# Optimization experiments

Measured on AMD Instinct MI355X. Metric: run time of the kernel, lower is better.

## Reference

```python
import jax, jax.numpy as jnp
import numpy as np
import math

D_MODEL = 1024
N_HEADS = 16
HEAD_DIM = D_MODEL // N_HEADS
B, T = 2, 2048


def _rope(q, k):
    # q, k: (B, H, T, Dh)
    Dh = q.shape[-1]
    Tq = q.shape[2]
    dim = jnp.arange(0, Dh, 2, dtype=jnp.float32)
    inv_freq = 1.0 / (10000.0 ** (dim / Dh))
    pos = jnp.arange(Tq, dtype=jnp.float32)
    freqs = pos[:, None] * inv_freq[None, :]          # (T, Dh/2)
    sin = jnp.sin(freqs)[None, None]                  # (1,1,T,Dh/2)
    cos = jnp.cos(freqs)[None, None]

    def rot(t):
        te, to = t[..., ::2], t[..., 1::2]
        re = te * cos - to * sin
        ro = te * sin + to * cos
        return jnp.stack([re, ro], axis=-1).reshape(t.shape)

    return rot(q), rot(k)


def setup_inputs() -> dict:
    key = jax.random.key(0)
    ks = jax.random.split(key, 4)
    std = 1.0 / math.sqrt(D_MODEL)
    x = jax.random.normal(ks[0], (B, T, D_MODEL), dtype=jnp.float32)
    W_qkv = jax.random.normal(ks[1], (D_MODEL, 3 * D_MODEL), dtype=jnp.float32) * std
    b_qkv = jnp.zeros((3 * D_MODEL,), dtype=jnp.float32)
    W_out = jax.random.normal(ks[2], (D_MODEL, D_MODEL), dtype=jnp.float32) * std
    b_out = jnp.zeros((D_MODEL,), dtype=jnp.float32)
    attention_mask = jnp.ones((B, T), dtype=jnp.int32)
    return {"x": x, "attention_mask": attention_mask, "W_qkv": W_qkv,
            "b_qkv": b_qkv, "W_out": W_out, "b_out": b_out}


def reference(x, attention_mask, W_qkv, b_qkv, W_out, b_out):
    Bx, Tx, D = x.shape
    qkv = x @ W_qkv + b_qkv                            # (B,T,3D)
    q, k, v = jnp.split(qkv, 3, axis=-1)
    # (B,T,H,Dh) -> (B,H,T,Dh)
    q = q.reshape(Bx, Tx, N_HEADS, HEAD_DIM).transpose(0, 2, 1, 3)
    k = k.reshape(Bx, Tx, N_HEADS, HEAD_DIM).transpose(0, 2, 1, 3)
    v = v.reshape(Bx, Tx, N_HEADS, HEAD_DIM).transpose(0, 2, 1, 3)
    q, k = _rope(q, k)
    scale = 1.0 / math.sqrt(float(HEAD_DIM))
    scores = jnp.einsum('bhqd,bhkd->bhqk', q, k) * scale
    causal = jnp.tril(jnp.ones((Tx, Tx), dtype=bool))[None, None]
    pad = attention_mask.astype(bool)[:, None, None, :]
    mask = causal & pad
    scores = jnp.where(mask, scores, -jnp.inf)
    probs = jax.nn.softmax(scores, axis=-1)
    out = jnp.einsum('bhqk,bhkd->bhqd', probs, v)      # (B,H,T,Dh)
    out = out.transpose(0, 2, 1, 3).reshape(Bx, Tx, D)
    return out @ W_out + b_out
```

## Files before the change

### kernel.cpp

```cpp
#include <hip/hip_runtime.h>
#include <math.h>
#include <stdint.h>

#define D_MODEL 1024
#define N_HEADS 16
#define HEAD_DIM 64
#define BATCH 2
#define SEQ 2048
#define TOKENS (BATCH * SEQ)

typedef __attribute__((ext_vector_type(8))) short short8;
typedef __attribute__((ext_vector_type(8))) _Float16 half8;
typedef __attribute__((ext_vector_type(4))) float floatx4;

#define BMFMA(a, b, c) __builtin_amdgcn_mfma_f32_16x16x32_bf16(a, b, c, 0, 0, 0)
#define HMFMA(a, b, c) __builtin_amdgcn_mfma_f32_16x16x32_f16(a, b, c, 0, 0, 0)

__device__ __forceinline__ unsigned short f2bf(float f) {
    uint32_t u = __float_as_uint(f);
    u += 0x7fffu + ((u >> 16) & 1u);
    return (unsigned short)(u >> 16);
}
__device__ __forceinline__ float bf2f(unsigned short h) {
    return __uint_as_float(((uint32_t)h) << 16);
}
__device__ __forceinline__ unsigned short f2h(float f) {
    union { _Float16 h; unsigned short u; } cv;
    cv.h = (_Float16)f;
    return cv.u;
}
__device__ __forceinline__ float h2f(unsigned short u) {
    union { unsigned short u; _Float16 h; } cv;
    cv.u = u;
    return (float)cv.h;
}

#define GLD_LDS16(gp, lp) __builtin_amdgcn_global_load_lds(                 \
    (const __attribute__((address_space(1))) void*)(gp),                    \
    (__attribute__((address_space(3))) void*)(lp), 16, 0, 0)

__global__ __launch_bounds__(256) void split_inputs(
    const float* __restrict__ X, const float* __restrict__ Wqkv,
    const float* __restrict__ Wout, const int* __restrict__ am,
    unsigned short* __restrict__ Axh, unsigned short* __restrict__ Bt,
    unsigned short* __restrict__ Bt2, unsigned long long* __restrict__ mbits,
    float2* __restrict__ tab)
{
    __shared__ float t[32][33];
    const int tid = threadIdx.x;
    const int bid = blockIdx.x;
    if (bid < 2048) {
        const int idx = bid * 2048 + tid * 8;
        const int row = idx >> 10;
        const int c = idx & 1023;
        float4 v0 = *(const float4*)(X + (size_t)row * 1024 + c);
        float4 v1 = *(const float4*)(X + (size_t)row * 1024 + c + 4);
        float f[8] = {v0.x, v0.y, v0.z, v0.w, v1.x, v1.y, v1.z, v1.w};
        uint32_t p[4];
#pragma unroll
        for (int j = 0; j < 4; ++j)
            p[j] = (uint32_t)f2h(f[2 * j]) | ((uint32_t)f2h(f[2 * j + 1]) << 16);
        *(uint4*)(Axh + (size_t)row * 1024 + c) = *(uint4*)p;
    } else if (bid < 5120) {
        const int id = bid - 2048;
        const int n0 = (id % 96) * 32, k0 = (id / 96) * 32;
        const int c = tid & 31, r = tid >> 5;
#pragma unroll
        for (int i = 0; i < 4; ++i)
            t[r + 8 * i][c] = Wqkv[(size_t)(k0 + r + 8 * i) * 3072 + n0 + c];
        __syncthreads();
#pragma unroll
        for (int i = 0; i < 4; ++i) {
            int dn = r + 8 * i;
            Bt[(size_t)(n0 + dn) * 1024 + k0 + c] = f2h(t[c][dn]);
        }
    } else if (bid < 6144) {
        const int id = bid - 5120;
        const int n0 = (id & 31) * 32, k0 = (id >> 5) * 32;
        const int c = tid & 31, r = tid >> 5;
#pragma unroll
        for (int i = 0; i < 4; ++i)
            t[r + 8 * i][c] = Wout[(size_t)(k0 + r + 8 * i) * 1024 + n0 + c];
        __syncthreads();
#pragma unroll
        for (int i = 0; i < 4; ++i) {
            int dn = r + 8 * i;
            Bt2[(size_t)(n0 + dn) * 1024 + k0 + c] = f2h(t[c][dn]);
        }
    } else if (bid == 6144) {
        if (tid < 64) {
            const int* a = am + tid * 64;
            unsigned long long m = 0ull;
            for (int j = 0; j < 64; ++j)
                m |= (unsigned long long)(a[j] != 0 ? 1u : 0u) << j;
            mbits[tid] = m;
        }
    } else {
        const int i = bid - 6145;
#pragma unroll
        for (int e = 0; e < 16; ++e) {
            int idx = i * 4096 + e * 256 + tid;
            int tt = idx >> 5, pr = idx & 31;
            double ex = (double)(2 * pr) / 64.0;
            float inv = (float)exp2(-ex * 13.287712379549449);
            float ang = (float)tt * inv;
            float s, c;
            __sincosf(ang, &s, &c);
            tab[idx] = make_float2(c, s);
        }
    }
}

__global__ __launch_bounds__(256) void gemm_qkv_fused(
    const unsigned short* __restrict__ Axh, const unsigned short* __restrict__ Bt,
    const float* __restrict__ bias, const float2* __restrict__ tab,
    unsigned short* __restrict__ Qh, unsigned short* __restrict__ Kh,
    unsigned short* __restrict__ Vh)
{
    __shared__ __align__(16) unsigned short sA0[4096], sA1[4096];
    __shared__ __align__(16) unsigned short sB0[4096], sB1[4096];

    const int tid = threadIdx.x;
    const int w = tid >> 6, lane = tid & 63;
    const int l15 = lane & 15, quad = lane >> 4;
    const int wm = w >> 1, wn = w & 1;

    const int lin = blockIdx.x;
    const int msuper = lin / 192;
    const int rem = lin % 192;
    const int m0 = (msuper * 8 + (rem & 7)) * 128;
    const int n0 = (rem >> 3) * 128;

    const int ch = (lane & 3) ^ ((lane >> 3) & 3);
    const int sw = (quad ^ ((l15 >> 1) & 3)) * 8;

    const unsigned short* aG[2];
    const unsigned short* bG[2];
#pragma unroll
    for (int i = 0; i < 2; ++i) {
        aG[i] = Axh + (size_t)(m0 + (w * 2 + i) * 16 + (lane >> 2)) * 1024 + ch * 8;
        bG[i] = Bt + (size_t)(n0 + (w * 2 + i) * 16 + (lane >> 2)) * 1024 + ch * 8;
    }

    floatx4 acc[4][4];
#pragma unroll
    for (int fm = 0; fm < 4; ++fm)
#pragma unroll
        for (int fn = 0; fn < 4; ++fn) acc[fm][fn] = (floatx4)0.f;

    for (int ks = 0; ks < 16; ++ks) {
        const int ko = ks * 64;
        __syncthreads();
#pragma unroll
        for (int i = 0; i < 2; ++i) {
            GLD_LDS16(aG[i] + ko,      sA0 + (w * 2 + i) * 512);
            GLD_LDS16(aG[i] + ko + 32, sA1 + (w * 2 + i) * 512);
            GLD_LDS16(bG[i] + ko,      sB0 + (w * 2 + i) * 512);
            GLD_LDS16(bG[i] + ko + 32, sB1 + (w * 2 + i) * 512);
        }
        __syncthreads();

        half8 a0[4], a1[4], b0[4], b1[4];
#pragma unroll
        for (int fm = 0; fm < 4; ++fm) {
            const int off = ((wm * 4 + fm) * 16 + l15) * 32 + sw;
            a0[fm] = *(const half8*)&sA0[off];
            a1[fm] = *(const half8*)&sA1[off];
        }
#pragma unroll
        for (int fn = 0; fn < 4; ++fn) {
            const int off = ((wn * 4 + fn) * 16 + l15) * 32 + sw;
            b0[fn] = *(const half8*)&sB0[off];
            b1[fn] = *(const half8*)&sB1[off];
        }
#pragma unroll
        for (int fm = 0; fm < 4; ++fm)
#pragma unroll
            for (int fn = 0; fn < 4; ++fn) {
                floatx4 a = acc[fm][fn];
                a = HMFMA(a0[fm], b0[fn], a);
                a = HMFMA(a1[fm], b1[fn], a);
                acc[fm][fn] = a;
            }
    }

    if (n0 < 2048) {
        const bool isQ = (n0 < 1024);
        unsigned short* dst = isQ ? Qh : Kh;
        const float qs = isQ ? 0.125f : 1.0f;
#pragma unroll
        for (int fm = 0; fm < 4; ++fm)
#pragma unroll
            for (int fn = 0; fn < 4; ++fn) {
                const int col = n0 + (wn * 4 + fn) * 16 + l15;
                const int hcol = col & 1023;
                const int hh = hcol >> 6, d = hcol & 63;
                const int pr = d >> 1;
                const bool odd = (d & 1) != 0;
                const float bv = bias[col];
#pragma unroll
                for (int r = 0; r < 4; ++r) {
                    const int row = m0 + (wm * 4 + fm) * 16 + quad * 4 + r;
                    const int tg = row & 2047, bb = row >> 11;
                    float val = acc[fm][fn][r] + bv;
                    float part = __shfl_xor(val, 1);
                    const float2 cs = tab[tg * 32 + pr];
                    float res = odd ? (part * cs.y + val * cs.x)
                                    : (val * cs.x - part * cs.y);
                    dst[((size_t)(bb * 16 + hh) * SEQ + tg) * 64 + d] =
                        f2h(res * qs);
                }
            }
    } else {
#pragma unroll
        for (int fm = 0; fm < 4; ++fm)
#pragma unroll
            for (int fn = 0; fn < 4; ++fn) {
                const int col = n0 + (wn * 4 + fn) * 16 + l15;
                const int hcol = col & 1023;
                const int hh = hcol >> 6, d = hcol & 63;
                const float bv = bias[col];
                const int row0 = m0 + (wm * 4 + fm) * 16 + quad * 4;
                const int tg0 = row0 & 2047, bb = row0 >> 11;
                uint32_t pk0 = (uint32_t)f2bf(acc[fm][fn][0] + bv)
                             | ((uint32_t)f2bf(acc[fm][fn][1] + bv) << 16);
                uint32_t pk1 = (uint32_t)f2bf(acc[fm][fn][2] + bv)
                             | ((uint32_t)f2bf(acc[fm][fn][3] + bv) << 16);
                *(uint2*)(Vh + ((size_t)(bb * 16 + hh) * 64 + d) * SEQ + tg0) =
                    make_uint2(pk0, pk1);
            }
    }
}

template<int WM, int WN, int FM, int FN>
__global__ __launch_bounds__(256) void gemm_mfma_h(
    const unsigned short* __restrict__ A, int lda,
    const unsigned short* __restrict__ Bt, int ldb,
    const float* __restrict__ bias, float* __restrict__ C, int ldc, int nTiles)
{
    constexpr int BM = WM * FM * 16;
    constexpr int BN = WN * FN * 16;
    constexpr int NA = BM / 64;
    constexpr int NB = BN / 64;

    __shared__ __align__(16) unsigned short sA0[BM * 32];
    __shared__ __align__(16) unsigned short sA1[BM * 32];
    __shared__ __align__(16) unsigned short sB0[BN * 32];
    __shared__ __align__(16) unsigned short sB1[BN * 32];

    const int tid = threadIdx.x;
    const int w = tid >> 6, lane = tid & 63;
    const int l15 = lane & 15, quad = lane >> 4;
    const int wm = w / WN, wn = w % WN;

    const int lin = blockIdx.x;
    const int msuper = lin / (8 * nTiles);
    const int rem = lin % (8 * nTiles);
    const int m0 = (msuper * 8 + (rem & 7)) * BM;
    const int n0 = (rem >> 3) * BN;

    const int ch = (lane & 3) ^ ((lane >> 3) & 3);
    const int sw = (quad ^ ((l15 >> 1) & 3)) * 8;

    const unsigned short* aG[NA];
    const unsigned short* bG[NB];
#pragma unroll
    for (int i = 0; i < NA; ++i)
        aG[i] = A + (size_t)(m0 + (w * NA + i) * 16 + (lane >> 2)) * lda + ch * 8;
#pragma unroll
    for (int i = 0; i < NB; ++i)
        bG[i] = Bt + (size_t)(n0 + (w * NB + i) * 16 + (lane >> 2)) * ldb + ch * 8;

    floatx4 acc[FM][FN];
#pragma unroll
    for (int fm = 0; fm < FM; ++fm)
#pragma unroll
        for (int fn = 0; fn < FN; ++fn) acc[fm][fn] = (floatx4)0.f;

    for (int ks = 0; ks < 16; ++ks) {
        const int ko = ks * 64;
        __syncthreads();
#pragma unroll
        for (int i = 0; i < NA; ++i) {
            GLD_LDS16(aG[i] + ko,      sA0 + (w * NA + i) * 512);
            GLD_LDS16(aG[i] + ko + 32, sA1 + (w * NA + i) * 512);
        }
#pragma unroll
        for (int i = 0; i < NB; ++i) {
            GLD_LDS16(bG[i] + ko,      sB0 + (w * NB + i) * 512);
            GLD_LDS16(bG[i] + ko + 32, sB1 + (w * NB + i) * 512);
        }
        __syncthreads();

        half8 a0[FM], a1[FM], b0[FN], b1[FN];
#pragma unroll
        for (int fm = 0; fm < FM; ++fm) {
            const int off = ((wm * FM + fm) * 16 + l15) * 32 + sw;
            a0[fm] = *(const half8*)&sA0[off];
            a1[fm] = *(const half8*)&sA1[off];
        }
#pragma unroll
        for (int fn = 0; fn < FN; ++fn) {
            const int off = ((wn * FN + fn) * 16 + l15) * 32 + sw;
            b0[fn] = *(const half8*)&sB0[off];
            b1[fn] = *(const half8*)&sB1[off];
        }
#pragma unroll
        for (int fm = 0; fm < FM; ++fm)
#pragma unroll
            for (int fn = 0; fn < FN; ++fn) {
                floatx4 a = acc[fm][fn];
                a = HMFMA(a0[fm], b0[fn], a);
                a = HMFMA(a1[fm], b1[fn], a);
                acc[fm][fn] = a;
            }
    }

#pragma unroll
    for (int fm = 0; fm < FM; ++fm)
#pragma unroll
        for (int fn = 0; fn < FN; ++fn) {
            int col = n0 + (wn * FN + fn) * 16 + l15;
            float bv = bias[col];
#pragma unroll
            for (int r = 0; r < 4; ++r) {
                int row = m0 + (wm * FM + fm) * 16 + quad * 4 + r;
                C[(size_t)row * ldc + col] = acc[fm][fn][r] + bv;
            }
        }
}

__global__ __launch_bounds__(256, 6) void flash_mfma(
    const unsigned short* __restrict__ Qh, const unsigned short* __restrict__ Kh,
    const unsigned short* __restrict__ Vh,
    const unsigned long long* __restrict__ mbits,
    unsigned short* __restrict__ attnx,
    float* __restrict__ Opart, float* __restrict__ lpart)
{
    __shared__ __align__(16) unsigned short sK[4096];
    __shared__ __align__(16) unsigned short sV[4096];
    __shared__ __align__(16) unsigned short sP[4096];

    const int tid = threadIdx.x;
    const int lane = tid & 63, w = tid >> 6;
    const int l15 = lane & 15, quad = lane >> 4;
    const int lin0 = blockIdx.x;
    const int xcd = lin0 & 7, idx = lin0 >> 3;
    const int bh = xcd * 4 + (idx & 3);
    const int rank = idx >> 2;
    int qt, k0, kend, mode;
    if (rank < 16)        { qt = 16 + rank; k0 = 0;  kend = 15; mode = 1; }
    else {
        const int i = (rank - 16) >> 1;
        if ((rank & 1) == 0) { qt = 31 - i; k0 = 16; kend = qt; mode = 2; }
        else                 { qt = 15 - i; k0 = 0;  kend = qt; mode = 0; }
    }
    const int b = bh >> 4, h = bh & 15;
    const int sw = (quad ^ ((l15 >> 1) & 3)) * 8;
    const int ch = (lane & 3) ^ ((lane >> 3) & 3);
    unsigned short* pbase = sP + w * 1024;

    short8 ones;
#pragma unroll
    for (int jj = 0; jj < 8; ++jj) ones[jj] = (short)0x3F80;

    const size_t qb = ((size_t)bh * SEQ + qt * 64 + w * 16 + l15) * 64 + quad * 8;
    const half8 qh0 = *(const half8*)(Qh + qb);
    const half8 qh1 = *(const half8*)(Qh + qb + 32);

    unsigned int mlo = 0xffffffffu, mhi = 0xffffffffu;
    if (lane < 32) {
        unsigned long long mw = mbits[b * 32 + lane];
        mlo = (unsigned int)mw;
        mhi = (unsigned int)(mw >> 32);
    }
    const bool fullmask =
        (__ballot((mlo & mhi) == 0xffffffffu) == ~0ull);

    const size_t kRow0 = ((size_t)bh * SEQ + w * 16 + (lane >> 2)) * 64 + ch * 8;
    const size_t vRow  = ((size_t)bh * 64 + w * 16 + (lane >> 2)) * SEQ + ch * 8;

    floatx4 O[4];
    floatx4 lAcc = (floatx4)0.f;
#pragma unroll
    for (int nf = 0; nf < 4; ++nf) O[nf] = (floatx4)0.f;

    const int mg = qt * 64 + w * 16 + l15;

    for (int kt = k0; kt <= kend; ++kt) {
        __syncthreads();
        {
            const size_t kg = kRow0 + (size_t)kt * 64 * 64;
            const size_t vg = vRow + (size_t)kt * 64;
            GLD_LDS16(Kh + kg,      sK + w * 512);
            GLD_LDS16(Kh + kg + 32, sK + 2048 + w * 512);
            GLD_LDS16(Vh + vg,      sV + w * 512);
            GLD_LDS16(Vh + vg + 32, sV + 2048 + w * 512);
        }
        __syncthreads();

        const bool diag = (kt == qt);
        unsigned int wlo = 0xffffffffu, whi = 0xffffffffu;
        if (!fullmask) {
            wlo = (unsigned int)__shfl((int)mlo, kt);
            whi = (unsigned int)__shfl((int)mhi, kt);
        }

#pragma unroll
        for (int nf = 0; nf < 4; ++nf) {
            const int base = (nf * 16 + l15) * 32 + sw;
            const half8 k0v = *(const half8*)&sK[base];
            const half8 k1v = *(const half8*)&sK[2048 + base];
            floatx4 s = (floatx4)0.f;
            s = HMFMA(k0v, qh0, s);
            s = HMFMA(k1v, qh1, s);

            float pv[4];
            if (fullmask && !diag) {
#pragma unroll
                for (int r = 0; r < 4; ++r)
                    pv[r] = __expf(s[r] - 16.0f);
            } else {
                const int tb = kt * 64 + nf * 16 + quad * 4;
                const unsigned int msel = (nf & 2) ? whi : wlo;
                const int p4 = (nf & 1) * 16 + quad * 4;
#pragma unroll
                for (int r = 0; r < 4; ++r) {
                    bool ok = ((msel >> (p4 + r)) & 1u) != 0u;
                    if (diag) ok = ok && (tb + r <= mg);
                    pv[r] = ok ? __expf(s[r] - 16.0f) : 0.0f;
                }
            }
            uint32_t w0, w1;
            asm("v_cvt_pk_bf16_f32 %0, %1, %2" : "=v"(w0) : "v"(pv[0]), "v"(pv[1]));
            asm("v_cvt_pk_bf16_f32 %0, %1, %2" : "=v"(w1) : "v"(pv[2]), "v"(pv[3]));
            const int pos = (((nf & 1) * 2 + (quad >> 1)) ^ ((l15 >> 1) & 3));
            *(uint2*)(pbase + (nf >> 1) * 512 + l15 * 32 + pos * 8
                      + (quad & 1) * 4) = make_uint2(w0, w1);
        }

        const short8 pf0 = *(const short8*)(pbase + l15 * 32 + sw);
        const short8 pf1 = *(const short8*)(pbase + 512 + l15 * 32 + sw);

        lAcc = BMFMA(pf0, ones, lAcc);
        lAcc = BMFMA(pf1, ones, lAcc);
#pragma unroll
        for (int nf = 0; nf < 4; ++nf) {
            const int vb = (nf * 16 + l15) * 32 + sw;
            floatx4 o = O[nf];
            o = BMFMA(pf0, *(const short8*)&sV[vb], o);
            o = BMFMA(pf1, *(const short8*)&sV[2048 + vb], o);
            O[nf] = o;
        }
    }

    if (mode == 0) {
        float rl[4];
#pragma unroll
        for (int r = 0; r < 4; ++r) rl[r] = 1.0f / lAcc[r];
#pragma unroll
        for (int nf = 0; nf < 4; ++nf)
#pragma unroll
            for (int r = 0; r < 4; ++r) {
                const int tok = b * SEQ + qt * 64 + w * 16 + quad * 4 + r;
                const int col = h * 64 + nf * 16 + l15;
                attnx[(size_t)tok * 1024 + col] = f2h(O[nf][r] * rl[r]);
            }
    } else {
        const int qt16 = qt - 16;
        float* Op = Opart + ((mode == 2) ? 2097152 : 0)
                  + (((size_t)bh * 16 + qt16) * 64) * 64;
#pragma unroll
        for (int nf = 0; nf < 4; ++nf)
#pragma unroll
            for (int r = 0; r < 4; ++r)
                Op[(w * 16 + quad * 4 + r) * 64 + nf * 16 + l15] = O[nf][r];
        if (l15 == 0) {
            float* lp = lpart + ((mode == 2) ? 32768 : 0)
                      + (bh * 16 + qt16) * 64;
#pragma unroll
            for (int r = 0; r < 4; ++r)
                lp[w * 16 + quad * 4 + r] = lAcc[r];
        }
    }
}

__global__ __launch_bounds__(256) void flash_merge(
    const float* __restrict__ Opart, const float* __restrict__ lpart,
    unsigned short* __restrict__ attnx)
{
    const int bh = blockIdx.x >> 4, qt16 = blockIdx.x & 15;
    const int b = bh >> 4, h = bh & 15;
    const int tid = threadIdx.x;
    const int q = tid >> 2, dblk = (tid & 3) * 16;
    const size_t ob = (((size_t)bh * 16 + qt16) * 64 + q) * 64 + dblk;
    const int lb = (bh * 16 + qt16) * 64 + q;
    const float rl = 1.0f / (lpart[lb] + lpart[lb + 32768]);

    uint32_t ph[8];
#pragma unroll
    for (int i = 0; i < 4; ++i) {
        float4 a = *(const float4*)(Opart + ob + 4 * i);
        float4 c = *(const float4*)(Opart + ob + 2097152 + 4 * i);
        float f0 = (a.x + c.x) * rl, f1 = (a.y + c.y) * rl;
        float f2 = (a.z + c.z) * rl, f3 = (a.w + c.w) * rl;
        ph[2 * i]     = (uint32_t)f2h(f0) | ((uint32_t)f2h(f1) << 16);
        ph[2 * i + 1] = (uint32_t)f2h(f2) | ((uint32_t)f2h(f3) << 16);
    }
    const int tok = b * SEQ + (16 + qt16) * 64 + q;
    unsigned short* dst = attnx + (size_t)tok * 1024 + h * 64 + dblk;
    *(uint4*)dst = *(uint4*)&ph[0];
    *(uint4*)(dst + 8) = *(uint4*)&ph[4];
}

extern "C" void kernel_launch(void* const* d_in, const int* in_sizes, int n_in,
                              void* d_out, int out_size, void* d_ws, size_t ws_size,
                              hipStream_t stream)
{
    const float* x    = (const float*)d_in[0];
    const int*   am   = (const int*)d_in[1];
    const float* Wqkv = (const float*)d_in[2];
    const float* bqkv = (const float*)d_in[3];
    const float* Wout = (const float*)d_in[4];
    const float* bout = (const float*)d_in[5];
    float* out = (float*)d_out;

    char* ws = (char*)d_ws;
    unsigned short* Bt  = (unsigned short*)ws;
    unsigned short* Bt2 = (unsigned short*)(ws + 6291456);
    float2* tab = (float2*)(ws + 8388608);
    unsigned long long* mbits = (unsigned long long*)(ws + 8912896);
    unsigned short* attnx = (unsigned short*)(ws + 12582912);
    unsigned short* Qh = (unsigned short*)(ws + 62914560);
    unsigned short* Kh = (unsigned short*)(ws + 71303168);
    unsigned short* Vh = (unsigned short*)(ws + 79691776);
    unsigned short* Axh = (unsigned short*)(ws + 88080384);
    float* Opart = (float*)(ws + 88080384);
    float* lpart = (float*)(ws + 104857600);

    split_inputs<<<6161, 256, 0, stream>>>(x, Wqkv, Wout, am,
                                           Axh, Bt, Bt2, mbits, tab);

    gemm_qkv_fused<<<768, 256, 0, stream>>>(Axh, Bt, bqkv, tab, Qh, Kh, Vh);

    flash_mfma<<<1536, 256, 0, stream>>>(Qh, Kh, Vh, mbits, attnx,
                                         Opart, lpart);
    flash_merge<<<512, 256, 0, stream>>>(Opart, lpart, attnx);

    gemm_mfma_h<2, 2, 4, 4><<<256, 256, 0, stream>>>(
        attnx, 1024, Bt2, 1024, bout, out, 1024, 8);
}
```

Before: 185.1 us.

## Fuse split-KV merge into flash kernel via atomic counters; remap GEMM tiles per XCD

Removes the separate flash_merge launch. The second of the two split-KV blocks to finish, detected with an atomic counter after a threadfence, now reads its partner's partial output and row sum and writes the normalized result directly. Both GEMMs also change block-to-tile mapping so that blockIdx mod 8 picks a contiguous slab of tiles, which is meant to improve L2 locality per XCD on MI355X. This adds an atomic, a fence and extra syncthreads in the flash epilogue, and counters are reset in split_inputs each call.

```diff
diff --git a/kernel.cpp b/kernel.cpp
--- a/kernel.cpp
+++ b/kernel.cpp
@@ -44,7 +44,7 @@
     const float* __restrict__ Wout, const int* __restrict__ am,
     unsigned short* __restrict__ Axh, unsigned short* __restrict__ Bt,
     unsigned short* __restrict__ Bt2, unsigned long long* __restrict__ mbits,
-    float2* __restrict__ tab)
+    float2* __restrict__ tab, int* __restrict__ flags)
 {
     __shared__ float t[32][33];
     const int tid = threadIdx.x;
@@ -95,6 +95,8 @@
                 m |= (unsigned long long)(a[j] != 0 ? 1u : 0u) << j;
             mbits[tid] = m;
         }
+        flags[tid] = 0;
+        flags[tid + 256] = 0;
     } else {
         const int i = bid - 6145;
 #pragma unroll
@@ -126,10 +128,10 @@
     const int wm = w >> 1, wn = w & 1;
 
     const int lin = blockIdx.x;
-    const int msuper = lin / 192;
-    const int rem = lin % 192;
-    const int m0 = (msuper * 8 + (rem & 7)) * 128;
-    const int n0 = (rem >> 3) * 128;
+    const int s = lin & 7;
+    const int loc = lin >> 3;
+    const int m0 = ((s >> 1) * 8 + loc / 12) * 128;
+    const int n0 = ((s & 1) * 12 + loc % 12) * 128;
 
     const int ch = (lane & 3) ^ ((lane >> 3) & 3);
     const int sw = (quad ^ ((l15 >> 1) & 3)) * 8;
@@ -236,7 +238,8 @@
 __global__ __launch_bounds__(256) void gemm_mfma_h(
     const unsigned short* __restrict__ A, int lda,
     const unsigned short* __restrict__ Bt, int ldb,
-    const float* __restrict__ bias, float* __restrict__ C, int ldc, int nTiles)
+    const float* __restrict__ bias, float* __restrict__ C, int ldc,
+    int mPerSlab, int nTilesN)
 {
     constexpr int BM = WM * FM * 16;
     constexpr int BN = WN * FN * 16;
@@ -254,10 +257,9 @@
     const int wm = w / WN, wn = w % WN;
 
     const int lin = blockIdx.x;
-    const int msuper = lin / (8 * nTiles);
-    const int rem = lin % (8 * nTiles);
-    const int m0 = (msuper * 8 + (rem & 7)) * BM;
-    const int n0 = (rem >> 3) * BN;
+    const int s = lin & 7, loc = lin >> 3;
+    const int m0 = (s * mPerSlab + loc / nTilesN) * BM;
+    const int n0 = (loc % nTilesN) * BN;
 
     const int ch = (lane & 3) ^ ((lane >> 3) & 3);
     const int sw = (quad ^ ((l15 >> 1) & 3)) * 8;
@@ -335,11 +337,13 @@
     const unsigned short* __restrict__ Vh,
     const unsigned long long* __restrict__ mbits,
     unsigned short* __restrict__ attnx,
-    float* __restrict__ Opart, float* __restrict__ lpart)
+    float* __restrict__ Opart, float* __restrict__ lpart,
+    int* __restrict__ flags)
 {
     __shared__ __align__(16) unsigned short sK[4096];
     __shared__ __align__(16) unsigned short sV[4096];
     __shared__ __align__(16) unsigned short sP[4096];
+    __shared__ int sOld;
 
     const int tid = threadIdx.x;
     const int lane = tid & 63, w = tid >> 6;
@@ -468,8 +472,8 @@
             }
     } else {
         const int qt16 = qt - 16;
-        float* Op = Opart + ((mode == 2) ? 2097152 : 0)
-                  + (((size_t)bh * 16 + qt16) * 64) * 64;
+        const size_t obase = (((size_t)bh * 16 + qt16) * 64) * 64;
+        float* Op = Opart + ((mode == 2) ? 2097152 : 0) + obase;
 #pragma unroll
         for (int nf = 0; nf < 4; ++nf)
 #pragma unroll
@@ -482,35 +486,30 @@
             for (int r = 0; r < 4; ++r)
                 lp[w * 16 + quad * 4 + r] = lAcc[r];
         }
-    }
-}
-
-__global__ __launch_bounds__(256) void flash_merge(
-    const float* __restrict__ Opart, const float* __restrict__ lpart,
-    unsigned short* __restrict__ attnx)
-{
-    const int bh = blockIdx.x >> 4, qt16 = blockIdx.x & 15;
-    const int b = bh >> 4, h = bh & 15;
-    const int tid = threadIdx.x;
-    const int q = tid >> 2, dblk = (tid & 3) * 16;
-    const size_t ob = (((size_t)bh * 16 + qt16) * 64 + q) * 64 + dblk;
-    const int lb = (bh * 16 + qt16) * 64 + q;
-    const float rl = 1.0f / (lpart[lb] + lpart[lb + 32768]);
-
-    uint32_t ph[8];
-#pragma unroll
-    for (int i = 0; i < 4; ++i) {
-        float4 a = *(const float4*)(Opart + ob + 4 * i);
-        float4 c = *(const float4*)(Opart + ob + 2097152 + 4 * i);
-        float f0 = (a.x + c.x) * rl, f1 = (a.y + c.y) * rl;
-        float f2 = (a.z + c.z) * rl, f3 = (a.w + c.w) * rl;
-        ph[2 * i]     = (uint32_t)f2h(f0) | ((uint32_t)f2h(f1) << 16);
-        ph[2 * i + 1] = (uint32_t)f2h(f2) | ((uint32_t)f2h(f3) << 16);
-    }
-    const int tok = b * SEQ + (16 + qt16) * 64 + q;
-    unsigned short* dst = attnx + (size_t)tok * 1024 + h * 64 + dblk;
-    *(uint4*)dst = *(uint4*)&ph[0];
-    *(uint4*)(dst + 8) = *(uint4*)&ph[4];
+        __threadfence();
+        __syncthreads();
+        if (tid == 0) sOld = atomicAdd(&flags[bh * 16 + qt16], 1);
+        __syncthreads();
+        if (sOld == 1) {
+            const float* Oo = Opart + ((mode == 2) ? 0 : 2097152) + obase;
+            const float* lo = lpart + ((mode == 2) ? 0 : 32768)
+                            + (bh * 16 + qt16) * 64;
+            float rl[4];
+#pragma unroll
+            for (int r = 0; r < 4; ++r)
+                rl[r] = 1.0f / (lAcc[r] + lo[w * 16 + quad * 4 + r]);
+#pragma unroll
+            for (int nf = 0; nf < 4; ++nf)
+#pragma unroll
+                for (int r = 0; r < 4; ++r) {
+                    const int tok = b * SEQ + qt * 64 + w * 16 + quad * 4 + r;
+                    const int col = h * 64 + nf * 16 + l15;
+                    float v = O[nf][r]
+                            + Oo[(w * 16 + quad * 4 + r) * 64 + nf * 16 + l15];
+                    attnx[(size_t)tok * 1024 + col] = f2h(v * rl[r]);
+                }
+        }
+    }
 }
 
 extern "C" void kernel_launch(void* const* d_in, const int* in_sizes, int n_in,
@@ -537,16 +536,16 @@
     unsigned short* Axh = (unsigned short*)(ws + 88080384);
     float* Opart = (float*)(ws + 88080384);
     float* lpart = (float*)(ws + 104857600);
+    int* flags = (int*)(ws + 104857600 + 262144);
 
     split_inputs<<<6161, 256, 0, stream>>>(x, Wqkv, Wout, am,
-                                           Axh, Bt, Bt2, mbits, tab);
+                                           Axh, Bt, Bt2, mbits, tab, flags);
 
     gemm_qkv_fused<<<768, 256, 0, stream>>>(Axh, Bt, bqkv, tab, Qh, Kh, Vh);
 
     flash_mfma<<<1536, 256, 0, stream>>>(Qh, Kh, Vh, mbits, attnx,
-                                         Opart, lpart);
-    flash_merge<<<512, 256, 0, stream>>>(Opart, lpart, attnx);
+                                         Opart, lpart, flags);
 
     gemm_mfma_h<2, 2, 4, 4><<<256, 256, 0, stream>>>(
-        attnx, 1024, Bt2, 1024, bout, out, 1024, 8);
-}
+        attnx, 1024, Bt2, 1024, bout, out, 1024, 4, 8);
+}
```

After: 306.1 us. +65.4%, slower.
